# Performance work log

Hardware: AMD Instinct MI355X
Metric: run time of the kernel (lower is better)

The kernel has to match this reference:

```python
import jax, jax.numpy as jnp
import numpy as np

N_NODES = 131072
N_DST = 16384        # batch_size * num_supernodes = 8 * 2048
DEG = 16
N_EDGES = N_DST * DEG
IN_DIM, HID, NDIM = 3, 256, 2
POS_STD = 1.0


def _linear_params(key, fan_in, fan_out):
    # xavier_uniform weights, zero bias; torch Linear stores W as [out, in]
    limit = np.sqrt(6.0 / (fan_in + fan_out)).astype(np.float32)
    w = jax.random.uniform(key, (fan_out, fan_in), jnp.float32, -limit, limit)
    return w, jnp.zeros((fan_out,), jnp.float32)


def setup_inputs() -> dict:
    key = jax.random.key(0)
    ks = jax.random.split(key, 12)
    x = jax.random.normal(ks[0], (N_NODES, IN_DIM), jnp.float32)
    mesh_pos = jax.random.uniform(ks[1], (N_NODES, NDIM), jnp.float32)
    # dst column sorted, each supernode id 0..N_DST-1 appears DEG times (segment_csr layout)
    dst = jnp.repeat(jnp.arange(N_DST, dtype=jnp.int64), DEG)
    src = jax.random.randint(ks[2], (N_EDGES,), 0, N_NODES, jnp.int64)
    mesh_edges = jnp.stack([dst, src], axis=1)  # [E, 2] = (dst, src)
    batch_idx = jnp.repeat(jnp.arange(8, dtype=jnp.int64), N_NODES // 8)
    ip_w1, ip_b1 = _linear_params(ks[3], IN_DIM, HID)
    ip_w2, ip_b2 = _linear_params(ks[4], HID, HID)
    ip_w3, ip_b3 = _linear_params(ks[5], HID, HID)
    msg_w1, msg_b1 = _linear_params(ks[6], 2 * HID, 2 * HID)
    msg_w2, msg_b2 = _linear_params(ks[7], 2 * HID, HID)
    msg_w3, msg_b3 = _linear_params(ks[8], HID, HID)
    b_fourier = jax.random.normal(ks[9], (HID // 2, NDIM), jnp.float32) * POS_STD
    return {
        "x": x, "mesh_pos": mesh_pos, "mesh_edges": mesh_edges, "batch_idx": batch_idx,
        "ip_w1": ip_w1, "ip_b1": ip_b1, "ip_w2": ip_w2, "ip_b2": ip_b2,
        "ip_w3": ip_w3, "ip_b3": ip_b3, "b_fourier": b_fourier,
        "msg_w1": msg_w1, "msg_b1": msg_b1, "msg_w2": msg_w2, "msg_b2": msg_b2,
        "msg_w3": msg_w3, "msg_b3": msg_b3,
        "batch_size": 8, "num_supernodes": 2048,
    }


def reference(x, mesh_pos, mesh_edges, batch_idx,
              ip_w1, ip_b1, ip_w2, ip_b2, ip_w3, ip_b3, b_fourier,
              msg_w1, msg_b1, msg_w2, msg_b2, msg_w3, msg_b3,
              batch_size, num_supernodes):
    gelu = lambda t: jax.nn.gelu(t, approximate=False)  # torch nn.GELU default (erf)
    # input_proj MLP
    h = gelu(x @ ip_w1.T + ip_b1)
    h = gelu(h @ ip_w2.T + ip_b2)
    h = h @ ip_w3.T + ip_b3
    # gaussian sincos positional embedding
    proj = (2.0 * jnp.pi) * (mesh_pos @ b_fourier.T)  # [N, HID/2]
    h = h + jnp.concatenate([jnp.cos(proj), jnp.sin(proj)], axis=-1)
    # edge gather + concat + message MLP
    dst, src = mesh_edges[:, 0], mesh_edges[:, 1]
    m = jnp.concatenate([h[src], h[dst]], axis=1)  # [E, 2*HID]
    m = gelu(m @ msg_w1.T + msg_b1)
    m = gelu(m @ msg_w2.T + msg_b2)
    m = m @ msg_w3.T + msg_b3
    # segment mean over (sorted, compact) destination supernodes
    num_dst = batch_size * num_supernodes
    sums = jax.ops.segment_sum(m, dst, num_segments=num_dst)
    counts = jax.ops.segment_sum(jnp.ones((dst.shape[0],), m.dtype), dst, num_segments=num_dst)
    out = sums / jnp.maximum(counts, 1.0)[:, None]
    return out.reshape(batch_size, num_supernodes, out.shape[-1])
```

## Files before the change

kernel.cpp:

```cpp
#include <hip/hip_runtime.h>
#include <math.h>

#define N_NODES 131072
#define N_DST   16384
#define DEG     16
#define HID     256
#define N_EDGES 262144

typedef __bf16 bf16_8 __attribute__((ext_vector_type(8)));
typedef float  f32_4  __attribute__((ext_vector_type(4)));

__device__ __forceinline__ float gelu_f(float v) {
    float u = fmaf(v * v, -0.10294324f, -2.30220819f) * v;
    float e;
    asm("v_exp_f32 %0, %1" : "=v"(e) : "v"(u));
    return v * __builtin_amdgcn_rcpf(1.0f + e);
}
__device__ __forceinline__ f32_4 zero4() {
    f32_4 z; z[0] = 0.f; z[1] = 0.f; z[2] = 0.f; z[3] = 0.f; return z;
}

__device__ __forceinline__ void load_lds16(const __bf16* g, __bf16* l) {
    __builtin_amdgcn_global_load_lds(
        (__attribute__((address_space(1))) void*)g,
        (__attribute__((address_space(3))) void*)l, 16, 0, 0);
}

__global__ void prep_kernel(__bf16* __restrict__ out,
                            const float* __restrict__ w2,
                            const float* __restrict__ w3,
                            const float* __restrict__ mw1,
                            const float* __restrict__ mw2,
                            const float* __restrict__ mw3) {
    int i = blockIdx.x * 256 + threadIdx.x;
    if (i >= 589824) return;
    float v;
    if      (i <  65536) v = w2[i];
    else if (i < 131072) v = w3[i - 65536];
    else if (i < 393216) v = mw1[i - 131072];
    else if (i < 524288) v = mw2[i - 393216];
    else                 v = mw3[i - 524288];
    out[i] = (__bf16)v;
}

__global__ __launch_bounds__(256, 2) void enc123_kernel(
    const float* __restrict__ x, const float* __restrict__ ew1,
    const float* __restrict__ eb1, __bf16* __restrict__ hA,
    const __bf16* __restrict__ W2, const float* __restrict__ b2,
    const __bf16* __restrict__ W3, const float* __restrict__ b3,
    const float* __restrict__ pos, const float* __restrict__ bfour)
{
    __shared__ __align__(16) __bf16 sH[64 * 256];
    __shared__ __align__(16) __bf16 sB[16384];

    const int tid = threadIdx.x;
    const int m0  = blockIdx.x * 64;
    const int wave = tid >> 6, lane = tid & 63, ln = lane & 15, quad = lane >> 4;
    const int wm = wave >> 1, wn = wave & 1;

    auto stage_w = [&](const __bf16* W, int kb) {
        #pragma unroll
        for (int i = 0; i < 8; i++) {
            int idx = i * 256 + tid;
            int row = idx >> 3, kg = (idx & 7) ^ (row & 7);
            load_lds16(W + (size_t)row * 256 + kb * 64 + kg * 8, &sB[idx * 8]);
        }
    };

    stage_w(W2, 0);
    {
        const int c8 = tid & 31;
        const int rl = tid >> 5;
        float w[24], bb[8];
        #pragma unroll
        for (int i = 0; i < 6; i++) *(float4*)&w[i * 4] = ((const float4*)ew1)[c8 * 6 + i];
        *(float4*)&bb[0] = ((const float4*)eb1)[c8 * 2 + 0];
        *(float4*)&bb[4] = ((const float4*)eb1)[c8 * 2 + 1];
        #pragma unroll
        for (int rr = 0; rr < 8; rr++) {
            int row = rr * 8 + rl;
            int g = m0 + row;
            float x0 = x[g * 3 + 0], x1 = x[g * 3 + 1], x2 = x[g * 3 + 2];
            bf16_8 o;
            #pragma unroll
            for (int j = 0; j < 8; j++) {
                float v = fmaf(x2, w[j * 3 + 2],
                          fmaf(x1, w[j * 3 + 1],
                          fmaf(x0, w[j * 3 + 0], bb[j])));
                o[j] = (__bf16)gelu_f(v);
            }
            *(bf16_8*)&sH[row * 256 + ((c8 ^ (row & 7)) * 8)] = o;
        }
    }
    __syncthreads();

    f32_4 acc[2][8];
    #pragma unroll
    for (int i = 0; i < 2; i++)
        #pragma unroll
        for (int j = 0; j < 8; j++) acc[i][j] = zero4();

    #pragma unroll
    for (int kb = 0; kb < 4; kb++) {
        #pragma unroll
        for (int ks = 0; ks < 2; ks++) {
            int c = ks * 4 + quad;
            bf16_8 af[2], bfr[8];
            #pragma unroll
            for (int mt = 0; mt < 2; mt++) {
                int mr = wm * 32 + mt * 16 + ln;
                af[mt] = *(const bf16_8*)&sH[mr * 256 + ((kb * 8 + (c ^ (mr & 7))) * 8)];
            }
            #pragma unroll
            for (int nt = 0; nt < 8; nt++) {
                int nr = wn * 128 + nt * 16 + ln;
                bfr[nt] = *(const bf16_8*)&sB[nr * 64 + ((c ^ (nr & 7)) * 8)];
            }
            #pragma unroll
            for (int mt = 0; mt < 2; mt++)
                #pragma unroll
                for (int nt = 0; nt < 8; nt++)
                    acc[mt][nt] = __builtin_amdgcn_mfma_f32_16x16x32_bf16(af[mt], bfr[nt], acc[mt][nt], 0, 0, 0);
        }
        __syncthreads();
        if (kb < 3) {
            stage_w(W2, kb + 1);
            __syncthreads();
        }
    }
    stage_w(W3, 0);
    #pragma unroll
    for (int nt = 0; nt < 8; nt++) {
        int col = wn * 128 + nt * 16 + ln;
        float bb = b2[col];
        #pragma unroll
        for (int mt = 0; mt < 2; mt++) {
            #pragma unroll
            for (int r = 0; r < 4; r++) {
                int row = wm * 32 + mt * 16 + quad * 4 + r;
                sH[row * 256 + ((col + row * 8) & 255)] = (__bf16)gelu_f(acc[mt][nt][r] + bb);
            }
        }
    }
    #pragma unroll
    for (int i = 0; i < 2; i++)
        #pragma unroll
        for (int j = 0; j < 8; j++) acc[i][j] = zero4();
    __syncthreads();

    #pragma unroll
    for (int kb = 0; kb < 4; kb++) {
        #pragma unroll
        for (int ks = 0; ks < 2; ks++) {
            int c = ks * 4 + quad;
            int k0 = kb * 64 + ks * 32 + quad * 8;
            bf16_8 af[2], bfr[8];
            #pragma unroll
            for (int mt = 0; mt < 2; mt++) {
                int mr = wm * 32 + mt * 16 + ln;
                af[mt] = *(const bf16_8*)&sH[mr * 256 + ((k0 + mr * 8) & 255)];
            }
            #pragma unroll
            for (int nt = 0; nt < 8; nt++) {
                int nr = wn * 128 + nt * 16 + ln;
                bfr[nt] = *(const bf16_8*)&sB[nr * 64 + ((c ^ (nr & 7)) * 8)];
            }
            #pragma unroll
            for (int mt = 0; mt < 2; mt++)
                #pragma unroll
                for (int nt = 0; nt < 8; nt++)
                    acc[mt][nt] = __builtin_amdgcn_mfma_f32_16x16x32_bf16(af[mt], bfr[nt], acc[mt][nt], 0, 0, 0);
        }
        __syncthreads();
        if (kb < 3) {
            stage_w(W3, kb + 1);
            __syncthreads();
        }
    }
    __bf16* buf = sB + wave * 4096;
    float b3r[8], Bc0[8], Bc1[8];
    #pragma unroll
    for (int nt = 0; nt < 8; nt++) {
        int col = wn * 128 + nt * 16 + ln;
        b3r[nt] = b3[col];
        int jm = col & 127;
        Bc0[nt] = bfour[jm * 2 + 0];
        Bc1[nt] = bfour[jm * 2 + 1];
    }
    const bool iscos = (wn == 0);
    #pragma unroll
    for (int mt = 0; mt < 2; mt++) {
        #pragma unroll
        for (int r = 0; r < 4; r++) {
            int rowL = mt * 16 + quad * 4 + r;
            int rowE = m0 + wm * 32 + rowL;
            float p0 = pos[rowE * 2 + 0], p1 = pos[rowE * 2 + 1];
            #pragma unroll
            for (int nt = 0; nt < 8; nt++) {
                float f = 6.2831853071795864f * fmaf(p1, Bc1[nt], p0 * Bc0[nt]);
                float v = acc[mt][nt][r] + b3r[nt] + (iscos ? __cosf(f) : __sinf(f));
                int colL = nt * 16 + ln;
                buf[rowL * 128 + ((colL + rowL * 8) & 127)] = (__bf16)v;
            }
        }
    }
    #pragma unroll
    for (int p = 0; p < 8; p++) {
        int rowL = p * 4 + (lane >> 4);
        int c8 = lane & 15;
        bf16_8 vv = *(const bf16_8*)&buf[rowL * 128 + ((c8 * 8 + rowL * 8) & 127)];
        *(bf16_8*)&hA[(size_t)(m0 + wm * 32 + rowL) * 256 + wn * 128 + c8 * 8] = vv;
    }
}

__global__ __launch_bounds__(512, 1) void msg_fused(
    const __bf16* __restrict__ h, const int* __restrict__ edges,
    const __bf16* __restrict__ W1a, const __bf16* __restrict__ dmat,
    const __bf16* __restrict__ W2, const float* __restrict__ b2,
    __bf16* __restrict__ p2)
{
    __shared__ __align__(16) __bf16 sH[32768];
    __shared__ __align__(16) __bf16 sB[2][16384];
    __shared__ __align__(16) __bf16 sM1[16384];

    const int tid = threadIdx.x;
    const int e0  = blockIdx.x * 128;
    const int wave = tid >> 6, lane = tid & 63, ln = lane & 15, quad = lane >> 4;
    const int wm = wave >> 1, wn = wave & 1;

    int* s_src = (int*)sM1;
    if (tid < 128) s_src[tid] = edges[2 * (e0 + tid) + 1];
    __syncthreads();

    auto stage_w1 = [&](int q, int kb, int p) {
        const __bf16* s0 = W1a + (size_t)(q * 128) * 512 + kb * 128;
        #pragma unroll
        for (int i = 0; i < 4; i++) {
            int idx = i * 512 + tid;
            int r = idx >> 4, kg = (idx & 15) ^ (r & 7);
            load_lds16(s0 + r * 512 + kg * 8, &sB[p][idx * 8]);
        }
    };
    auto stage_w2 = [&](int q, int kb2, int p) {
        const __bf16* s0 = W2 + q * 128 + kb2 * 64;
        #pragma unroll
        for (int i = 0; i < 4; i++) {
            int idx = i * 512 + tid;
            int r = idx >> 3, kg = (idx & 7) ^ (r & 7);
            load_lds16(s0 + (size_t)r * 512 + kg * 8, &sB[p][idx * 8]);
        }
    };

    #pragma unroll
    for (int i = 0; i < 8; i++) {
        int idx = i * 512 + tid;
        int row = idx >> 5, kg = (idx & 31) ^ (row & 7);
        load_lds16(h + (size_t)s_src[row] * 256 + kg * 8, &sH[idx * 8]);
    }
    stage_w1(0, 0, 0);
    __syncthreads();

    f32_4 acc2[2][8];
    #pragma unroll
    for (int i = 0; i < 2; i++)
        #pragma unroll
        for (int j = 0; j < 8; j++) acc2[i][j] = zero4();

    #pragma unroll 1
    for (int q = 0; q < 4; q++) {
        const int colbase = q * 128 + wn * 64;
        float bd[2][4];
        #pragma unroll
        for (int nt = 0; nt < 4; nt++) {
            #pragma unroll
            for (int mt = 0; mt < 2; mt++) {
                int gid = blockIdx.x * 8 + wm * 2 + mt;
                bd[mt][nt] = (float)dmat[(size_t)gid * 512 + colbase + nt * 16 + ln];
            }
        }
        f32_4 acc1[2][4];
        #pragma unroll
        for (int i = 0; i < 2; i++)
            #pragma unroll
            for (int j = 0; j < 4; j++) acc1[i][j] = zero4();

        stage_w1(q, 1, 1);
        #pragma unroll
        for (int ks = 0; ks < 4; ks++) {
            int c = ks * 4 + quad;
            bf16_8 af[2], bfr[4];
            #pragma unroll
            for (int mt = 0; mt < 2; mt++) {
                int mr = wm * 32 + mt * 16 + ln;
                af[mt] = *(const bf16_8*)&sH[mr * 256 + ((c ^ (mr & 7)) * 8)];
            }
            #pragma unroll
            for (int nt = 0; nt < 4; nt++) {
                int nr = wn * 64 + nt * 16 + ln;
                bfr[nt] = *(const bf16_8*)&sB[0][nr * 128 + ((c ^ (nr & 7)) * 8)];
            }
            __builtin_amdgcn_s_setprio(1);
            #pragma unroll
            for (int mt = 0; mt < 2; mt++)
                #pragma unroll
                for (int nt = 0; nt < 4; nt++)
                    acc1[mt][nt] = __builtin_amdgcn_mfma_f32_16x16x32_bf16(af[mt], bfr[nt], acc1[mt][nt], 0, 0, 0);
            __builtin_amdgcn_s_setprio(0);
        }
        __syncthreads();

        stage_w2(q, 0, 0);
        #pragma unroll
        for (int ks = 0; ks < 4; ks++) {
            int cb = ks * 4 + quad;
            int ca = 16 + cb;
            bf16_8 af[2], bfr[4];
            #pragma unroll
            for (int mt = 0; mt < 2; mt++) {
                int mr = wm * 32 + mt * 16 + ln;
                af[mt] = *(const bf16_8*)&sH[mr * 256 + ((ca ^ (mr & 7)) * 8)];
            }
            #pragma unroll
            for (int nt = 0; nt < 4; nt++) {
                int nr = wn * 64 + nt * 16 + ln;
                bfr[nt] = *(const bf16_8*)&sB[1][nr * 128 + ((cb ^ (nr & 7)) * 8)];
            }
            __builtin_amdgcn_s_setprio(1);
            #pragma unroll
            for (int mt = 0; mt < 2; mt++)
                #pragma unroll
                for (int nt = 0; nt < 4; nt++)
                    acc1[mt][nt] = __builtin_amdgcn_mfma_f32_16x16x32_bf16(af[mt], bfr[nt], acc1[mt][nt], 0, 0, 0);
            __builtin_amdgcn_s_setprio(0);
        }
        #pragma unroll
        for (int mt = 0; mt < 2; mt++) {
            #pragma unroll
            for (int nt = 0; nt < 4; nt++) {
                #pragma unroll
                for (int r = 0; r < 4; r++) {
                    int row = wm * 32 + mt * 16 + quad * 4 + r;
                    int colq = wn * 64 + nt * 16 + ln;
                    float v = gelu_f(acc1[mt][nt][r] + bd[mt][nt]);
                    sM1[row * 128 + ((colq + row * 8) & 127)] = (__bf16)v;
                }
            }
        }
        __syncthreads();

        stage_w2(q, 1, 1);
        #pragma unroll
        for (int ks = 0; ks < 2; ks++) {
            int k0 = ks * 32 + quad * 8;
            int cb2 = ks * 4 + quad;
            bf16_8 af[2], bfr[8];
            #pragma unroll
            for (int mt = 0; mt < 2; mt++) {
                int mr = wm * 32 + mt * 16 + ln;
                af[mt] = *(const bf16_8*)&sM1[mr * 128 + ((k0 + mr * 8) & 127)];
            }
            #pragma unroll
            for (int nt = 0; nt < 8; nt++) {
                int nr = wn * 128 + nt * 16 + ln;
                bfr[nt] = *(const bf16_8*)&sB[0][nr * 64 + ((cb2 ^ (nr & 7)) * 8)];
            }
            __builtin_amdgcn_s_setprio(1);
            #pragma unroll
            for (int mt = 0; mt < 2; mt++)
                #pragma unroll
                for (int nt = 0; nt < 8; nt++)
                    acc2[mt][nt] = __builtin_amdgcn_mfma_f32_16x16x32_bf16(af[mt], bfr[nt], acc2[mt][nt], 0, 0, 0);
            __builtin_amdgcn_s_setprio(0);
        }
        __syncthreads();

        if (q < 3) stage_w1(q + 1, 0, 0);
        #pragma unroll
        for (int ks = 0; ks < 2; ks++) {
            int k0 = 64 + ks * 32 + quad * 8;
            int cb2 = ks * 4 + quad;
            bf16_8 af[2], bfr[8];
            #pragma unroll
            for (int mt = 0; mt < 2; mt++) {
                int mr = wm * 32 + mt * 16 + ln;
                af[mt] = *(const bf16_8*)&sM1[mr * 128 + ((k0 + mr * 8) & 127)];
            }
            #pragma unroll
            for (int nt = 0; nt < 8; nt++) {
                int nr = wn * 128 + nt * 16 + ln;
                bfr[nt] = *(const bf16_8*)&sB[1][nr * 64 + ((cb2 ^ (nr & 7)) * 8)];
            }
            __builtin_amdgcn_s_setprio(1);
            #pragma unroll
            for (int mt = 0; mt < 2; mt++)
                #pragma unroll
                for (int nt = 0; nt < 8; nt++)
                    acc2[mt][nt] = __builtin_amdgcn_mfma_f32_16x16x32_bf16(af[mt], bfr[nt], acc2[mt][nt], 0, 0, 0);
            __builtin_amdgcn_s_setprio(0);
        }
        __syncthreads();
    }

    #pragma unroll
    for (int nt = 0; nt < 8; nt++) {
        int col = wn * 128 + nt * 16 + ln;
        float bb = b2[col];
        #pragma unroll
        for (int mt = 0; mt < 2; mt++) {
            float s = gelu_f(acc2[mt][nt][0] + bb) + gelu_f(acc2[mt][nt][1] + bb)
                    + gelu_f(acc2[mt][nt][2] + bb) + gelu_f(acc2[mt][nt][3] + bb);
            s += __shfl_xor(s, 16);
            s += __shfl_xor(s, 32);
            if (quad == 0) {
                int dstn = edges[2 * (e0 + (wm * 2 + mt) * 16)];
                p2[(size_t)dstn * HID + col] = (__bf16)(s * 0.0625f);
            }
        }
    }
}

template<int K, int GMODE, int WLD, int WOFF, bool BIAS, bool POOL_, bool F32OUT>
__global__ __launch_bounds__(256, 3) void mgemm(
    const __bf16* __restrict__ Ag, const __bf16* __restrict__ h,
    const int* __restrict__ edges, const __bf16* __restrict__ W,
    const float* __restrict__ bias, __bf16* __restrict__ Cb,
    float* __restrict__ Cf, int NB, int Nfull, int e0)
{
    __shared__ __align__(16) __bf16 sA[128 * 64];
    __shared__ __align__(16) __bf16 sB[128 * 64];
    __shared__ int s_idx[128];

    const int tid  = threadIdx.x;
    const int mblk = blockIdx.x / NB;
    const int nblk = blockIdx.x % NB;
    const int m0 = mblk * 128, n0 = nblk * 128;
    const int wave = tid >> 6, lane = tid & 63, ln = lane & 15, quad = lane >> 4;
    const int wm = wave >> 1, wn = wave & 1;

    if (GMODE) {
        if (tid < 128) {
            int r = m0 + tid;
            s_idx[tid] = (GMODE == 1) ? edges[2 * (e0 + r) + 1]
                                      : edges[2 * (DEG * r)];
        }
        __syncthreads();
    }

    const __bf16* pA[4];
    const __bf16* pB[4];
    #pragma unroll
    for (int i = 0; i < 4; i++) {
        int idx = i * 256 + tid;
        int row = idx >> 3, kg = (idx & 7) ^ (row & 7);
        pA[i] = GMODE ? h + (size_t)s_idx[row] * HID + kg * 8
                      : Ag + (size_t)(m0 + row) * K + kg * 8;
        pB[i] = W + (size_t)(n0 + row) * WLD + WOFF + kg * 8;
    }
    const int ach = quad ^ (ln & 7);
    const int aof[2] = { (wm * 64 + ln) * 64 + ach * 8, (wm * 64 + ln) * 64 + (ach ^ 4) * 8 };
    const int bof[2] = { (wn * 64 + ln) * 64 + ach * 8, (wn * 64 + ln) * 64 + (ach ^ 4) * 8 };

    f32_4 acc[4][4];
    #pragma unroll
    for (int i = 0; i < 4; i++)
        #pragma unroll
        for (int j = 0; j < 4; j++) acc[i][j] = zero4();

    bf16_8 ar[4], br[4];
    #pragma unroll
    for (int i = 0; i < 4; i++) {
        ar[i] = *(const bf16_8*)pA[i];
        br[i] = *(const bf16_8*)pB[i];
    }

    #pragma unroll
    for (int kb = 0; kb < K / 64; kb++) {
        if (kb > 0) __syncthreads();
        #pragma unroll
        for (int i = 0; i < 4; i++) {
            int idx = i * 256 + tid;
            *(bf16_8*)&sA[idx * 8] = ar[i];
            *(bf16_8*)&sB[idx * 8] = br[i];
        }
        __syncthreads();
        if (kb + 1 < K / 64) {
            #pragma unroll
            for (int i = 0; i < 4; i++) {
                ar[i] = *(const bf16_8*)(pA[i] + (kb + 1) * 64);
                br[i] = *(const bf16_8*)(pB[i] + (kb + 1) * 64);
            }
        }
        #pragma unroll
        for (int ks = 0; ks < 2; ks++) {
            bf16_8 af[4], bfr[4];
            #pragma unroll
            for (int mt = 0; mt < 4; mt++) af[mt]  = *(const bf16_8*)&sA[aof[ks] + mt * 1024];
            #pragma unroll
            for (int nt = 0; nt < 4; nt++) bfr[nt] = *(const bf16_8*)&sB[bof[ks] + nt * 1024];
            #pragma unroll
            for (int mt = 0; mt < 4; mt++)
                #pragma unroll
                for (int nt = 0; nt < 4; nt++)
                    acc[mt][nt] = __builtin_amdgcn_mfma_f32_16x16x32_bf16(af[mt], bfr[nt], acc[mt][nt], 0, 0, 0);
        }
    }

    if (POOL_) {
        #pragma unroll
        for (int nt = 0; nt < 4; nt++) {
            int col = n0 + wn * 64 + nt * 16 + ln;
            float bb = BIAS ? bias[col] : 0.f;
            #pragma unroll
            for (int mt = 0; mt < 4; mt++) {
                float s = gelu_f(acc[mt][nt][0] + bb) + gelu_f(acc[mt][nt][1] + bb)
                        + gelu_f(acc[mt][nt][2] + bb) + gelu_f(acc[mt][nt][3] + bb);
                s += __shfl_xor(s, 16);
                s += __shfl_xor(s, 32);
                if (quad == 0) {
                    int eg  = e0 + m0 + wm * 64 + mt * 16;
                    int dstn = edges[2 * eg];
                    Cb[(size_t)dstn * HID + col] = (__bf16)(s * 0.0625f);
                }
            }
        }
    } else if (F32OUT) {
        #pragma unroll
        for (int nt = 0; nt < 4; nt++) {
            int col = n0 + wn * 64 + nt * 16 + ln;
            float bb = BIAS ? bias[col] : 0.f;
            #pragma unroll
            for (int mt = 0; mt < 4; mt++) {
                #pragma unroll
                for (int r = 0; r < 4; r++) {
                    int rowE = m0 + wm * 64 + mt * 16 + quad * 4 + r;
                    Cf[(size_t)rowE * Nfull + col] = acc[mt][nt][r] + bb;
                }
            }
        }
    } else {
        __syncthreads();
        __bf16* sw = ((wave & 2) ? sB : sA) + (wave & 1) * 4096;
        #pragma unroll
        for (int nt = 0; nt < 4; nt++) {
            float bb = BIAS ? bias[n0 + wn * 64 + nt * 16 + ln] : 0.f;
            #pragma unroll
            for (int mt = 0; mt < 4; mt++) {
                #pragma unroll
                for (int r = 0; r < 4; r++) {
                    int rowL = mt * 16 + quad * 4 + r;
                    int colL = nt * 16 + ln;
                    sw[rowL * 64 + ((colL + rowL * 8) & 63)] = (__bf16)(acc[mt][nt][r] + bb);
                }
            }
        }
        __syncthreads();
        #pragma unroll
        for (int p = 0; p < 8; p++) {
            int rowL = p * 8 + (lane >> 3);
            int c8 = lane & 7;
            bf16_8 vv = *(const bf16_8*)&sw[rowL * 64 + ((c8 * 8 + rowL * 8) & 63)];
            int rowE = m0 + wm * 64 + rowL;
            *(bf16_8*)&Cb[(size_t)rowE * Nfull + n0 + wn * 64 + c8 * 8] = vv;
        }
    }
}

extern "C" void kernel_launch(void* const* d_in, const int* in_sizes, int n_in,
                              void* d_out, int out_size, void* d_ws, size_t ws_size,
                              hipStream_t stream) {
    const float* x     = (const float*)d_in[0];
    const float* pos   = (const float*)d_in[1];
    const int*   edges = (const int*)d_in[2];
    const float* ip_w1 = (const float*)d_in[4];
    const float* ip_b1 = (const float*)d_in[5];
    const float* ip_w2 = (const float*)d_in[6];
    const float* ip_b2 = (const float*)d_in[7];
    const float* ip_w3 = (const float*)d_in[8];
    const float* ip_b3 = (const float*)d_in[9];
    const float* bfour = (const float*)d_in[10];
    const float* mw1   = (const float*)d_in[11];
    const float* mb1   = (const float*)d_in[12];
    const float* mw2   = (const float*)d_in[13];
    const float* mb2   = (const float*)d_in[14];
    const float* mw3   = (const float*)d_in[15];
    const float* mb3   = (const float*)d_in[16];

    char* ws = (char*)d_ws;
    __bf16* hA = (__bf16*)ws;
    size_t off = (size_t)N_NODES * HID * 2;
    __bf16* wb = (__bf16*)(ws + off);
    off += (size_t)589824 * 2;
    off = (off + 255) & ~(size_t)255;
    __bf16* dbuf = (__bf16*)(ws + off);
    off += (size_t)N_DST * 512 * 2;
    __bf16* p2 = (__bf16*)(ws + off);
    off += (size_t)N_DST * HID * 2;

    __bf16* w2b  = wb;
    __bf16* w3b  = wb + 65536;
    __bf16* mw1b = wb + 131072;
    __bf16* mw2b = wb + 393216;
    __bf16* mw3b = wb + 524288;

    prep_kernel<<<2304, 256, 0, stream>>>(wb, ip_w2, ip_w3, mw1, mw2, mw3);

    enc123_kernel<<<2048, 256, 0, stream>>>(x, ip_w1, ip_b1, hA,
                                            w2b, ip_b2, w3b, ip_b3, pos, bfour);

    mgemm<256, 2, 512, 256, true, false, false><<<512, 256, 0, stream>>>(
        nullptr, hA, edges, mw1b, mb1, dbuf, nullptr, 4, 512, 0);

    msg_fused<<<2048, 512, 0, stream>>>(hA, edges, mw1b, dbuf, mw2b, mb2, p2);

    mgemm<256, 0, 256, 0, true, false, true><<<256, 256, 0, stream>>>(
        p2, nullptr, nullptr, mw3b, mb3, nullptr, (float*)d_out, 2, 256, 0);
}
```

Before: 404.3 us.

## Double-buffer encoder weight staging in half-K slices and raise MFMA wave priority

The encoder's W2/W3 staging moves from one 64-wide K buffer, loaded between two barriers, to two 32-wide ping-pong buffers. The next slice's async global-to-LDS load is issued before computing on the current slice, leaving one barrier per step. This is meant to hide weight-load latency behind MFMA work and remove a barrier per iteration. It also wraps MFMA blocks in s_setprio raises in both the encoder and the message GEMM kernel, at the cost of more, smaller iterations and a new swizzle.

After: 404.0 us. Within noise of the previous version (-0.1%).

```diff
diff --git a/kernel.cpp b/kernel.cpp
--- a/kernel.cpp
+++ b/kernel.cpp
@@ -51,23 +51,24 @@
     const float* __restrict__ pos, const float* __restrict__ bfour)
 {
     __shared__ __align__(16) __bf16 sH[64 * 256];
-    __shared__ __align__(16) __bf16 sB[16384];
+    __shared__ __align__(16) __bf16 sBh[2][8192];
 
     const int tid = threadIdx.x;
     const int m0  = blockIdx.x * 64;
     const int wave = tid >> 6, lane = tid & 63, ln = lane & 15, quad = lane >> 4;
     const int wm = wave >> 1, wn = wave & 1;
 
-    auto stage_w = [&](const __bf16* W, int kb) {
-        #pragma unroll
-        for (int i = 0; i < 8; i++) {
+    auto stage_half = [&](const __bf16* W, int hs, int p) {
+        #pragma unroll
+        for (int i = 0; i < 4; i++) {
             int idx = i * 256 + tid;
-            int row = idx >> 3, kg = (idx & 7) ^ (row & 7);
-            load_lds16(W + (size_t)row * 256 + kb * 64 + kg * 8, &sB[idx * 8]);
+            int r = idx >> 2, sl = idx & 3;
+            int kg = sl ^ ((r >> 1) & 3);
+            load_lds16(W + (size_t)r * 256 + hs * 32 + kg * 8, &sBh[p][idx * 8]);
         }
     };
 
-    stage_w(W2, 0);
+    stage_half(W2, 0, 0);
     {
         const int c8 = tid & 31;
         const int rl = tid >> 5;
@@ -101,34 +102,33 @@
         for (int j = 0; j < 8; j++) acc[i][j] = zero4();
 
     #pragma unroll
-    for (int kb = 0; kb < 4; kb++) {
-        #pragma unroll
-        for (int ks = 0; ks < 2; ks++) {
-            int c = ks * 4 + quad;
+    for (int hs = 0; hs < 8; hs++) {
+        if (hs < 7) stage_half(W2, hs + 1, (hs + 1) & 1);
+        else        stage_half(W3, 0, 0);
+        {
+            int c = (hs & 1) * 4 + quad;
             bf16_8 af[2], bfr[8];
             #pragma unroll
             for (int mt = 0; mt < 2; mt++) {
                 int mr = wm * 32 + mt * 16 + ln;
-                af[mt] = *(const bf16_8*)&sH[mr * 256 + ((kb * 8 + (c ^ (mr & 7))) * 8)];
+                af[mt] = *(const bf16_8*)&sH[mr * 256 + (((hs >> 1) * 8 + (c ^ (mr & 7))) * 8)];
             }
             #pragma unroll
             for (int nt = 0; nt < 8; nt++) {
                 int nr = wn * 128 + nt * 16 + ln;
-                bfr[nt] = *(const bf16_8*)&sB[nr * 64 + ((c ^ (nr & 7)) * 8)];
-            }
+                int sl = quad ^ ((nr >> 1) & 3);
+                bfr[nt] = *(const bf16_8*)&sBh[hs & 1][nr * 32 + sl * 8];
+            }
+            __builtin_amdgcn_s_setprio(1);
             #pragma unroll
             for (int mt = 0; mt < 2; mt++)
                 #pragma unroll
                 for (int nt = 0; nt < 8; nt++)
                     acc[mt][nt] = __builtin_amdgcn_mfma_f32_16x16x32_bf16(af[mt], bfr[nt], acc[mt][nt], 0, 0, 0);
-        }
-        __syncthreads();
-        if (kb < 3) {
-            stage_w(W2, kb + 1);
-            __syncthreads();
-        }
-    }
-    stage_w(W3, 0);
+            __builtin_amdgcn_s_setprio(0);
+        }
+        __syncthreads();
+    }
     #pragma unroll
     for (int nt = 0; nt < 8; nt++) {
         int col = wn * 128 + nt * 16 + ln;
@@ -149,11 +149,10 @@
     __syncthreads();
 
     #pragma unroll
-    for (int kb = 0; kb < 4; kb++) {
-        #pragma unroll
-        for (int ks = 0; ks < 2; ks++) {
-            int c = ks * 4 + quad;
-            int k0 = kb * 64 + ks * 32 + quad * 8;
+    for (int hs = 0; hs < 8; hs++) {
+        if (hs < 7) stage_half(W3, hs + 1, (hs + 1) & 1);
+        {
+            int k0 = hs * 32 + quad * 8;
             bf16_8 af[2], bfr[8];
             #pragma unroll
             for (int mt = 0; mt < 2; mt++) {
@@ -163,21 +162,20 @@
             #pragma unroll
             for (int nt = 0; nt < 8; nt++) {
                 int nr = wn * 128 + nt * 16 + ln;
-                bfr[nt] = *(const bf16_8*)&sB[nr * 64 + ((c ^ (nr & 7)) * 8)];
-            }
+                int sl = quad ^ ((nr >> 1) & 3);
+                bfr[nt] = *(const bf16_8*)&sBh[hs & 1][nr * 32 + sl * 8];
+            }
+            __builtin_amdgcn_s_setprio(1);
             #pragma unroll
             for (int mt = 0; mt < 2; mt++)
                 #pragma unroll
                 for (int nt = 0; nt < 8; nt++)
                     acc[mt][nt] = __builtin_amdgcn_mfma_f32_16x16x32_bf16(af[mt], bfr[nt], acc[mt][nt], 0, 0, 0);
-        }
-        __syncthreads();
-        if (kb < 3) {
-            stage_w(W3, kb + 1);
-            __syncthreads();
-        }
-    }
-    __bf16* buf = sB + wave * 4096;
+            __builtin_amdgcn_s_setprio(0);
+        }
+        __syncthreads();
+    }
+    __bf16* buf = &sBh[0][0] + wave * 4096;
     float b3r[8], Bc0[8], Bc1[8];
     #pragma unroll
     for (int nt = 0; nt < 8; nt++) {
@@ -497,11 +495,13 @@
             for (int mt = 0; mt < 4; mt++) af[mt]  = *(const bf16_8*)&sA[aof[ks] + mt * 1024];
             #pragma unroll
             for (int nt = 0; nt < 4; nt++) bfr[nt] = *(const bf16_8*)&sB[bof[ks] + nt * 1024];
+            __builtin_amdgcn_s_setprio(1);
             #pragma unroll
             for (int mt = 0; mt < 4; mt++)
                 #pragma unroll
                 for (int nt = 0; nt < 4; nt++)
                     acc[mt][nt] = __builtin_amdgcn_mfma_f32_16x16x32_bf16(af[mt], bfr[nt], acc[mt][nt], 0, 0, 0);
+            __builtin_amdgcn_s_setprio(0);
         }
     }
 
```
